# Kernel tuning notes

Measured on AMD Instinct MI355X. Metric: run time of the kernel, lower is better.

## Reference

```python
import jax, jax.numpy as jnp
import numpy as np

EMBED_DIM = 512
N_HEADS = 8
HEAD_DIM = EMBED_DIM // N_HEADS
B, N = 4, 2048


def setup_inputs() -> dict:
    key = jax.random.key(0)
    ks = jax.random.split(key, 5)
    x = jax.random.normal(ks[0], (B, N, EMBED_DIM), dtype=jnp.float32)
    # torch Linear weights are (out, in); init scale ~ 1/sqrt(in)
    s = 1.0 / np.sqrt(EMBED_DIM)
    WQ = jax.random.uniform(ks[1], (EMBED_DIM, EMBED_DIM), jnp.float32, -s, s)
    WK = jax.random.uniform(ks[2], (EMBED_DIM, EMBED_DIM), jnp.float32, -s, s)
    WV = jax.random.uniform(ks[3], (EMBED_DIM, EMBED_DIM), jnp.float32, -s, s)
    WO = jax.random.uniform(ks[4], (EMBED_DIM, EMBED_DIM), jnp.float32, -s, s)
    mask = jnp.tril(jnp.ones((N, N), dtype=jnp.int32))  # causal mask
    return {"x": x, "WQ": WQ, "WK": WK, "WV": WV, "WO": WO, "mask": mask}


def reference(x, WQ, WK, WV, WO, mask):
    scale = HEAD_DIM ** -0.5
    # Linear: y = x @ W.T ; then split heads -> (B, H, N, Dh)
    def proj(W):
        y = jnp.einsum('bnd,ed->bne', x, W)
        return y.reshape(B, N, N_HEADS, HEAD_DIM).transpose(0, 2, 1, 3)
    Q, K, V = proj(WQ), proj(WK), proj(WV)
    scores = jnp.einsum('bhnd,bhmd->bhnm', Q, K) * scale  # (B,H,N,N)
    scores = jnp.where(mask[None, None, :, :] == 0, -jnp.inf, scores)
    attn = jax.nn.softmax(scores, axis=-1)
    # dropout is identity in eval mode
    out = jnp.einsum('bhnm,bhmd->bhnd', attn, V)
    out = out.transpose(0, 2, 1, 3).reshape(B, N, EMBED_DIM)
    return jnp.einsum('bne,de->bnd', out, WO)
```

## Files before the change

### kernel.cpp

```cpp
#include <hip/hip_runtime.h>
#include <hip/hip_bf16.h>

#define B_  4
#define N_  2048
#define E_  512
#define H_  8
#define DH_ 64
#define M_  (B_ * N_)

typedef __attribute__((ext_vector_type(8))) short bq8;
typedef __attribute__((ext_vector_type(4))) float f32x4;

#define QSCALE_ (0.125f * 1.44269504f)

static __device__ __forceinline__ unsigned short f2bf(float f) {
    unsigned u = __float_as_uint(f);
    unsigned r = (u + 0x7fffu + ((u >> 16) & 1u)) >> 16;
    return (unsigned short)r;
}
static __device__ __forceinline__ unsigned short f2bf_fast(float f) {
    return (unsigned short)((__float_as_uint(f) + 0x8000u) >> 16);
}

static __device__ __forceinline__ void gld_lds16(const unsigned short* g,
                                                 unsigned short* l)
{
    __builtin_amdgcn_global_load_lds(
        (const __attribute__((address_space(1))) void*)g,
        (__attribute__((address_space(3))) void*)l,
        16, 0, 0);
}

static __device__ __forceinline__ void cvt16(const void* src, unsigned short* dst,
                                             int base, bool isBf)
{
    if (isBf) {
        const uint4* s = (const uint4*)((const unsigned short*)src + base);
        uint4 a = s[0], b = s[1];
        *(uint4*)(dst + base)     = a;
        *(uint4*)(dst + base + 8) = b;
    } else {
        const float* s = (const float*)src + base;
        unsigned short tmp[16];
        #pragma unroll
        for (int c = 0; c < 16; c += 4) {
            const float4 v = *(const float4*)(s + c);
            tmp[c + 0] = f2bf(v.x); tmp[c + 1] = f2bf(v.y);
            tmp[c + 2] = f2bf(v.z); tmp[c + 3] = f2bf(v.w);
        }
        *(uint4*)(dst + base)     = *(uint4*)&tmp[0];
        *(uint4*)(dst + base + 8) = *(uint4*)&tmp[8];
    }
}

__global__ __launch_bounds__(256)
void cvt_all(const void* __restrict__ sx,
             const void* __restrict__ s0, const void* __restrict__ s1,
             const void* __restrict__ s2, const void* __restrict__ s3,
             unsigned short* __restrict__ dx,
             unsigned short* __restrict__ d0, unsigned short* __restrict__ d1,
             unsigned short* __restrict__ d2, unsigned short* __restrict__ d3,
             int* __restrict__ dflag)
{
    __shared__ int wtot[4];
    const int bid = blockIdx.x;
    const int t   = threadIdx.x;
    const void* s;
    unsigned short* d;
    int base;
    if (bid < 1024) {
        s = sx; d = dx;
        base = bid * 4096 + t * 16;
    } else {
        const int wb = bid - 1024;
        const int wi = wb >> 6;
        s = (wi == 0) ? s0 : (wi == 1) ? s1 : (wi == 2) ? s2 : s3;
        d = (wi == 0) ? d0 : (wi == 1) ? d1 : (wi == 2) ? d2 : d3;
        base = (wb & 63) * 4096 + t * 16;
    }

    const unsigned* sw = (const unsigned*)s;
    int cnt = 0;
    #pragma unroll
    for (int i = 0; i < 4; ++i) {
        const unsigned w = sw[t * 4 + i];
        const unsigned elo = (w >> 7) & 0xffu;
        const unsigned ehi = (w >> 23) & 0xffu;
        cnt += (elo >= 100u && elo <= 150u && ehi >= 100u && ehi <= 150u) ? 1 : 0;
    }
    cnt += __shfl_xor(cnt, 1);  cnt += __shfl_xor(cnt, 2);
    cnt += __shfl_xor(cnt, 4);  cnt += __shfl_xor(cnt, 8);
    cnt += __shfl_xor(cnt, 16); cnt += __shfl_xor(cnt, 32);
    if ((t & 63) == 0) wtot[t >> 6] = cnt;
    __syncthreads();
    const int total = wtot[0] + wtot[1] + wtot[2] + wtot[3];
    const bool isBf = (total >= 512);
    if (bid == 0 && t == 0) dflag[0] = isBf ? 1 : 0;

    cvt16(s, d, base, isBf);
}

template<int BN>
__global__ __launch_bounds__(256)
void gemm_bf16(const unsigned short* __restrict__ A,
               const unsigned short* __restrict__ W0,
               const unsigned short* __restrict__ W1,
               const unsigned short* __restrict__ W2,
               void* __restrict__ C0, void* __restrict__ C1, void* __restrict__ C2,
               const int* __restrict__ dflag, int cSel)
{
    constexpr int NB = BN / 32;
    __shared__ unsigned short As[128 * 32];
    __shared__ unsigned short Bs[BN * 32];

    const int extBf = dflag[0];
    const unsigned short* Wv = (blockIdx.z == 0) ? W0 : (blockIdx.z == 1) ? W1 : W2;
    void*                 Cv = (blockIdx.z == 0) ? C0 : (blockIdx.z == 1) ? C1 : C2;
    const int  mode  = (cSel == 1) ? 1 : ((blockIdx.z == 2) ? 2 : 0);
    const bool vswap = (mode == 2);
    const float qs = (cSel == 0 && blockIdx.z == 0) ? QSCALE_ : 1.0f;

    const int t    = threadIdx.x;
    const int w    = t >> 6;
    const int lane = t & 63;
    const int ln   = lane & 15;
    const int qd   = lane >> 4;
    const int wm   = w >> 1;
    const int wn   = w & 1;

    const int m0 = blockIdx.x * 128;
    const int n0 = blockIdx.y * BN;

    const int lr = lane >> 2;
    const int lc = (lane & 3) * 8;
    const unsigned short* gA0 = A + (size_t)(m0 + w * 32 + lr) * E_ + lc;
    const unsigned short* gA1 = gA0 + 16 * E_;
    unsigned short* lA0 = As + w * 32 * 32;
    unsigned short* lA1 = lA0 + 16 * 32;

    const unsigned short* gB0;
    const unsigned short* gB1 = nullptr;
    unsigned short* lB0;
    unsigned short* lB1 = nullptr;
    if (BN == 128) {
        gB0 = Wv + (size_t)(n0 + w * 32 + lr) * E_ + lc;
        gB1 = gB0 + 16 * E_;
        lB0 = Bs + w * 32 * 32;
        lB1 = lB0 + 16 * 32;
    } else {
        gB0 = Wv + (size_t)(n0 + w * 16 + lr) * E_ + lc;
        lB0 = Bs + w * 16 * 32;
    }

    f32x4 acc[4][4];
    #pragma unroll
    for (int i = 0; i < 4; ++i)
        #pragma unroll
        for (int j = 0; j < 4; ++j)
            acc[i][j] = (f32x4){0.f, 0.f, 0.f, 0.f};

    for (int k0 = 0; k0 < E_; k0 += 32) {
        __syncthreads();
        gld_lds16(gA0 + k0, lA0);
        gld_lds16(gA1 + k0, lA1);
        gld_lds16(gB0 + k0, lB0);
        if (BN == 128) gld_lds16(gB1 + k0, lB1);
        __syncthreads();

        bq8 afr[4], bfr[NB];
        #pragma unroll
        for (int i = 0; i < 4; ++i)
            afr[i] = *(const bq8*)&As[(wm * 64 + i * 16 + ln) * 32 + qd * 8];
        #pragma unroll
        for (int j = 0; j < NB; ++j)
            bfr[j] = *(const bq8*)&Bs[(wn * (BN / 2) + j * 16 + ln) * 32 + qd * 8];

        if (vswap) {
            #pragma unroll
            for (int i = 0; i < 4; ++i)
                #pragma unroll
                for (int j = 0; j < NB; ++j)
                    acc[i][j] = __builtin_amdgcn_mfma_f32_16x16x32_bf16(afr[i], bfr[j], acc[i][j], 0, 0, 0);
        } else {
            #pragma unroll
            for (int i = 0; i < NB; ++i)
                #pragma unroll
                for (int j = 0; j < 4; ++j)
                    acc[i][j] = __builtin_amdgcn_mfma_f32_16x16x32_bf16(bfr[i], afr[j], acc[i][j], 0, 0, 0);
        }
    }

    if (mode == 2) {
        unsigned short* C = (unsigned short*)Cv;
        const int colBase = n0 + wn * 64;
        const int hh = colBase >> 6;
        #pragma unroll
        for (int i = 0; i < 4; ++i) {
            const int token = m0 + wm * 64 + i * 16 + qd * 4;
            const int bb = token >> 11;
            const int nn = token & 2047;
            #pragma unroll
            for (int j = 0; j < 4; ++j) {
                const int d = j * 16 + ln;
                ushort4 o4;
                o4.x = f2bf(acc[i][j][0]);
                o4.y = f2bf(acc[i][j][1]);
                o4.z = f2bf(acc[i][j][2]);
                o4.w = f2bf(acc[i][j][3]);
                *(ushort4*)(C + ((size_t)(bb * H_ + hh) * 64 + d) * N_ + nn) = o4;
            }
        }
    } else if (mode == 0 || extBf) {
        unsigned short* C = (unsigned short*)Cv;
        #pragma unroll
        for (int i = 0; i < NB; ++i) {
            const int n = n0 + wn * (BN / 2) + i * 16 + qd * 4;
            #pragma unroll
            for (int j = 0; j < 4; ++j) {
                const int m = m0 + wm * 64 + j * 16 + ln;
                ushort4 o4;
                o4.x = f2bf(acc[i][j][0] * qs);
                o4.y = f2bf(acc[i][j][1] * qs);
                o4.z = f2bf(acc[i][j][2] * qs);
                o4.w = f2bf(acc[i][j][3] * qs);
                *(ushort4*)(C + (size_t)m * E_ + n) = o4;
            }
        }
    } else {
        float* C = (float*)Cv;
        #pragma unroll
        for (int i = 0; i < NB; ++i) {
            const int n = n0 + wn * (BN / 2) + i * 16 + qd * 4;
            #pragma unroll
            for (int j = 0; j < 4; ++j) {
                const int m = m0 + wm * 64 + j * 16 + ln;
                *(f32x4*)(C + (size_t)m * E_ + n) = acc[i][j];
            }
        }
    }
}

__global__ __launch_bounds__(256)
void attn_causal(const unsigned short* __restrict__ Q,
                 const unsigned short* __restrict__ K,
                 const unsigned short* __restrict__ VtG,
                 unsigned short* __restrict__ O)
{
    __shared__ unsigned short Ks[128 * 72];
    __shared__ unsigned short Vs[64 * 136];
    __shared__ unsigned short Pq[64 * 264];

    const int bx  = blockIdx.x;
    const int qlo = bx;
    const int qhi = 31 - bx;
    const int h   = blockIdx.y;
    const int b   = blockIdx.z;
    const int t   = threadIdx.x;
    const int w    = t >> 6;
    const int lane = t & 63;
    const int ln   = lane & 15;
    const int qd   = lane >> 4;

    const int CA = (qlo + 2) >> 1;
    const int CB = (qhi + 2) >> 1;

    const int col0 = h * DH_;
    const size_t rowBase = (size_t)b * N_;
    const unsigned short* Vhead = VtG + (size_t)(b * H_ + h) * 64 * N_;

    const int jbase = qd * 4;
    const int mloc  = w * 16 + ln;
    const int qAg = qlo * 64 + mloc;
    const int qBg = qhi * 64 + mloc;
    const int prow = mloc * 264;

    const unsigned short* Qa = Q + (rowBase + qAg) * E_ + col0 + qd * 8;
    const unsigned short* Qb = Q + (rowBase + qBg) * E_ + col0 + qd * 8;
    const bq8 qfA0 = *(const bq8*)(Qa);
    const bq8 qfA1 = *(const bq8*)(Qa + 32);
    const bq8 qfB0 = *(const bq8*)(Qb);
    const bq8 qfB1 = *(const bq8*)(Qb + 32);

    const int kr = t >> 1;
    const int kc = (t & 1) * 32;
    const int vr = t >> 2;
    const int vc = (t & 3) * 32;
    const unsigned short* gK = K + (rowBase + kr) * E_ + col0 + kc;
    const unsigned short* gV = Vhead + (size_t)vr * N_ + vc;

    float lA = 0.f, lB = 0.f;
    f32x4 oA[4], oB[4];
    #pragma unroll
    for (int dt = 0; dt < 4; ++dt) {
        oA[dt] = (f32x4){0.f, 0.f, 0.f, 0.f};
        oB[dt] = (f32x4){0.f, 0.f, 0.f, 0.f};
    }

    uint4 kR0, kR1, kR2, kR3, vR0, vR1, vR2, vR3;
    {
        const uint4* ks = (const uint4*)gK;
        kR0 = ks[0]; kR1 = ks[1]; kR2 = ks[2]; kR3 = ks[3];
        const uint4* vs = (const uint4*)gV;
        vR0 = vs[0]; vR1 = vs[1]; vR2 = vs[2]; vR3 = vs[3];
    }

    for (int kt = 0; kt < CB; ++kt) {
        const bool actA = (kt < CA);

        __syncthreads();
        *(uint4*)&Ks[kr * 72 + kc]      = kR0;
        *(uint4*)&Ks[kr * 72 + kc + 8]  = kR1;
        *(uint4*)&Ks[kr * 72 + kc + 16] = kR2;
        *(uint4*)&Ks[kr * 72 + kc + 24] = kR3;
        *(uint4*)&Vs[vr * 136 + vc]      = vR0;
        *(uint4*)&Vs[vr * 136 + vc + 8]  = vR1;
        *(uint4*)&Vs[vr * 136 + vc + 16] = vR2;
        *(uint4*)&Vs[vr * 136 + vc + 24] = vR3;
        __syncthreads();

        if (kt + 1 < CB) {
            const uint4* ks = (const uint4*)(gK + (size_t)(kt + 1) * 128 * E_);
            kR0 = ks[0]; kR1 = ks[1]; kR2 = ks[2]; kR3 = ks[3];
            const uint4* vs = (const uint4*)(gV + (kt + 1) * 128);
            vR0 = vs[0]; vR1 = vs[1]; vR2 = vs[2]; vR3 = vs[3];
        }

        const int gb = kt * 128 + jbase;

        f32x4 sA[8];
        const bool diagB = (kt == CB - 1);
        #pragma unroll
        for (int ct = 0; ct < 8; ++ct) {
            const bq8 kf0 = *(const bq8*)&Ks[(ct * 16 + ln) * 72 + qd * 8];
            const bq8 kf1 = *(const bq8*)&Ks[(ct * 16 + ln) * 72 + 32 + qd * 8];
            f32x4 c = (f32x4){0.f, 0.f, 0.f, 0.f};
            c = __builtin_amdgcn_mfma_f32_16x16x32_bf16(kf0, qfB0, c, 0, 0, 0);
            c = __builtin_amdgcn_mfma_f32_16x16x32_bf16(kf1, qfB1, c, 0, 0, 0);
            if (actA) {
                f32x4 ca = (f32x4){0.f, 0.f, 0.f, 0.f};
                ca = __builtin_amdgcn_mfma_f32_16x16x32_bf16(kf0, qfA0, ca, 0, 0, 0);
                ca = __builtin_amdgcn_mfma_f32_16x16x32_bf16(kf1, qfA1, ca, 0, 0, 0);
                sA[ct] = ca;
            }
            float p0 = exp2f(c[0]);
            float p1 = exp2f(c[1]);
            float p2 = exp2f(c[2]);
            float p3 = exp2f(c[3]);
            if (diagB) {
                const int kb = gb + ct * 16;
                if (kb + 0 > qBg) p0 = 0.f;
                if (kb + 1 > qBg) p1 = 0.f;
                if (kb + 2 > qBg) p2 = 0.f;
                if (kb + 3 > qBg) p3 = 0.f;
            }
            lB += (p0 + p1) + (p2 + p3);
            ushort4 pk;
            pk.x = f2bf_fast(p0); pk.y = f2bf_fast(p1);
            pk.z = f2bf_fast(p2); pk.w = f2bf_fast(p3);
            *(ushort4*)&Pq[prow + 136 + ct * 16 + jbase] = pk;
        }

        if (actA) {
            const bool diagA = (kt == CA - 1);
            #pragma unroll
            for (int ct = 0; ct < 8; ++ct) {
                float p0 = exp2f(sA[ct][0]);
                float p1 = exp2f(sA[ct][1]);
                float p2 = exp2f(sA[ct][2]);
                float p3 = exp2f(sA[ct][3]);
                if (diagA) {
                    const int kb = gb + ct * 16;
                    if (kb + 0 > qAg) p0 = 0.f;
                    if (kb + 1 > qAg) p1 = 0.f;
                    if (kb + 2 > qAg) p2 = 0.f;
                    if (kb + 3 > qAg) p3 = 0.f;
                }
                lA += (p0 + p1) + (p2 + p3);
                ushort4 pk;
                pk.x = f2bf_fast(p0); pk.y = f2bf_fast(p1);
                pk.z = f2bf_fast(p2); pk.w = f2bf_fast(p3);
                *(ushort4*)&Pq[prow + ct * 16 + jbase] = pk;
            }
        }

        {
            const bq8 pB0 = *(const bq8*)&Pq[prow + 136 + qd * 8];
            const bq8 pB1 = *(const bq8*)&Pq[prow + 136 + 32 + qd * 8];
            const bq8 pB2 = *(const bq8*)&Pq[prow + 136 + 64 + qd * 8];
            const bq8 pB3 = *(const bq8*)&Pq[prow + 136 + 96 + qd * 8];
            bq8 pA0, pA1, pA2, pA3;
            if (actA) {
                pA0 = *(const bq8*)&Pq[prow + qd * 8];
                pA1 = *(const bq8*)&Pq[prow + 32 + qd * 8];
                pA2 = *(const bq8*)&Pq[prow + 64 + qd * 8];
                pA3 = *(const bq8*)&Pq[prow + 96 + qd * 8];
            }
            __builtin_amdgcn_s_setprio(1);
            #pragma unroll
            for (int dt = 0; dt < 4; ++dt) {
                const int vb = (dt * 16 + ln) * 136;
                const bq8 vf0 = *(const bq8*)&Vs[vb + qd * 8];
                const bq8 vf1 = *(const bq8*)&Vs[vb + 32 + qd * 8];
                const bq8 vf2 = *(const bq8*)&Vs[vb + 64 + qd * 8];
                const bq8 vf3 = *(const bq8*)&Vs[vb + 96 + qd * 8];
                oB[dt] = __builtin_amdgcn_mfma_f32_16x16x32_bf16(vf0, pB0, oB[dt], 0, 0, 0);
                oB[dt] = __builtin_amdgcn_mfma_f32_16x16x32_bf16(vf1, pB1, oB[dt], 0, 0, 0);
                oB[dt] = __builtin_amdgcn_mfma_f32_16x16x32_bf16(vf2, pB2, oB[dt], 0, 0, 0);
                oB[dt] = __builtin_amdgcn_mfma_f32_16x16x32_bf16(vf3, pB3, oB[dt], 0, 0, 0);
                if (actA) {
                    oA[dt] = __builtin_amdgcn_mfma_f32_16x16x32_bf16(vf0, pA0, oA[dt], 0, 0, 0);
                    oA[dt] = __builtin_amdgcn_mfma_f32_16x16x32_bf16(vf1, pA1, oA[dt], 0, 0, 0);
                    oA[dt] = __builtin_amdgcn_mfma_f32_16x16x32_bf16(vf2, pA2, oA[dt], 0, 0, 0);
                    oA[dt] = __builtin_amdgcn_mfma_f32_16x16x32_bf16(vf3, pA3, oA[dt], 0, 0, 0);
                }
            }
            __builtin_amdgcn_s_setprio(0);
        }
    }

    lA += __shfl_xor(lA, 16); lA += __shfl_xor(lA, 32);
    lB += __shfl_xor(lB, 16); lB += __shfl_xor(lB, 32);
    const float invA = 1.f / lA;
    const float invB = 1.f / lB;

    unsigned short* oAp = O + (rowBase + qlo * 64 + mloc) * E_ + col0 + jbase;
    unsigned short* oBp = O + (rowBase + qhi * 64 + mloc) * E_ + col0 + jbase;
    #pragma unroll
    for (int dt = 0; dt < 4; ++dt) {
        ushort4 a4, b4;
        a4.x = f2bf(oA[dt][0] * invA); a4.y = f2bf(oA[dt][1] * invA);
        a4.z = f2bf(oA[dt][2] * invA); a4.w = f2bf(oA[dt][3] * invA);
        b4.x = f2bf(oB[dt][0] * invB); b4.y = f2bf(oB[dt][1] * invB);
        b4.z = f2bf(oB[dt][2] * invB); b4.w = f2bf(oB[dt][3] * invB);
        *(ushort4*)(oAp + dt * 16) = a4;
        *(ushort4*)(oBp + dt * 16) = b4;
    }
}

extern "C" void kernel_launch(void* const* d_in, const int* in_sizes, int n_in,
                              void* d_out, int out_size, void* d_ws, size_t ws_size,
                              hipStream_t stream)
{
    const void* x  = d_in[0];
    const void* WQ = d_in[1];
    const void* WK = d_in[2];
    const void* WV = d_in[3];
    const void* WO = d_in[4];

    int* dflag = (int*)d_ws;
    unsigned short* xb  = (unsigned short*)((char*)d_ws + 256);
    unsigned short* wqb = xb  + (size_t)M_ * E_;
    unsigned short* wkb = wqb + (size_t)E_ * E_;
    unsigned short* wvb = wkb + (size_t)E_ * E_;
    unsigned short* wob = wvb + (size_t)E_ * E_;
    unsigned short* q   = wob + (size_t)E_ * E_;
    unsigned short* k   = q   + (size_t)M_ * E_;
    unsigned short* v   = k   + (size_t)M_ * E_;
    unsigned short* o   = v   + (size_t)M_ * E_;

    cvt_all<<<1280, 256, 0, stream>>>(x, WQ, WK, WV, WO,
                                      xb, wqb, wkb, wvb, wob, dflag);

    gemm_bf16<128><<<dim3(M_ / 128, E_ / 128, 3), 256, 0, stream>>>(
        xb, wqb, wkb, wvb, q, k, v, dflag, 0);

    attn_causal<<<dim3(16, H_, B_), 256, 0, stream>>>(q, k, v, o);

    gemm_bf16<64><<<dim3(M_ / 128, E_ / 64, 1), 256, 0, stream>>>(
        o, wob, wob, wob, d_out, d_out, d_out, dflag, 1);
}
```

Before: 197.3 us.

## Specialize causal attention loop into paired and B-only paths, share P buffer

Splits the key-tile loop of the paired-tile causal attention kernel into two branches. One handles tiles where both the low and high query tiles are active, the other handles tiles where only the high tile remains, which removes the per-instruction actA predicates and the live sA array. The P staging buffer in LDS is halved by writing and reading A's probabilities first, then reusing the same rows for B, which lowers shared-memory use per block. Manual bf16 rounding is replaced by the packed v_cvt_pk_bf16_f32 instruction. The intent is fewer instructions, lower register and LDS pressure, and possibly higher occupancy, at the cost of duplicated code and a serialized write/read of P within the active path.

After: 174.9 us. 11.4% less time.

```diff
diff --git a/kernel.cpp b/kernel.cpp
--- a/kernel.cpp
+++ b/kernel.cpp
@@ -18,8 +18,11 @@
     unsigned r = (u + 0x7fffu + ((u >> 16) & 1u)) >> 16;
     return (unsigned short)r;
 }
-static __device__ __forceinline__ unsigned short f2bf_fast(float f) {
-    return (unsigned short)((__float_as_uint(f) + 0x8000u) >> 16);
+
+static __device__ __forceinline__ unsigned cvtpk_bf16(float lo, float hi) {
+    unsigned r;
+    asm("v_cvt_pk_bf16_f32 %0, %1, %2" : "=v"(r) : "v"(lo), "v"(hi));
+    return r;
 }
 
 static __device__ __forceinline__ void gld_lds16(const unsigned short* g,
@@ -248,7 +251,7 @@
 {
     __shared__ unsigned short Ks[128 * 72];
     __shared__ unsigned short Vs[64 * 136];
-    __shared__ unsigned short Pq[64 * 264];
+    __shared__ unsigned short Pq[64 * 136];
 
     const int bx  = blockIdx.x;
     const int qlo = bx;
@@ -272,7 +275,7 @@
     const int mloc  = w * 16 + ln;
     const int qAg = qlo * 64 + mloc;
     const int qBg = qhi * 64 + mloc;
-    const int prow = mloc * 264;
+    const int prow = mloc * 136;
 
     const unsigned short* Qa = Q + (rowBase + qAg) * E_ + col0 + qd * 8;
     const unsigned short* Qb = Q + (rowBase + qBg) * E_ + col0 + qd * 8;
@@ -305,8 +308,6 @@
     }
 
     for (int kt = 0; kt < CB; ++kt) {
-        const bool actA = (kt < CA);
-
         __syncthreads();
         *(uint4*)&Ks[kr * 72 + kc]      = kR0;
         *(uint4*)&Ks[kr * 72 + kc + 8]  = kR1;
@@ -327,47 +328,24 @@
 
         const int gb = kt * 128 + jbase;
 
-        f32x4 sA[8];
-        const bool diagB = (kt == CB - 1);
-        #pragma unroll
-        for (int ct = 0; ct < 8; ++ct) {
-            const bq8 kf0 = *(const bq8*)&Ks[(ct * 16 + ln) * 72 + qd * 8];
-            const bq8 kf1 = *(const bq8*)&Ks[(ct * 16 + ln) * 72 + 32 + qd * 8];
-            f32x4 c = (f32x4){0.f, 0.f, 0.f, 0.f};
-            c = __builtin_amdgcn_mfma_f32_16x16x32_bf16(kf0, qfB0, c, 0, 0, 0);
-            c = __builtin_amdgcn_mfma_f32_16x16x32_bf16(kf1, qfB1, c, 0, 0, 0);
-            if (actA) {
+        if (kt < CA) {
+            const bool diagA = (kt == CA - 1);
+            f32x4 sB[8];
+            #pragma unroll
+            for (int ct = 0; ct < 8; ++ct) {
+                const bq8 kf0 = *(const bq8*)&Ks[(ct * 16 + ln) * 72 + qd * 8];
+                const bq8 kf1 = *(const bq8*)&Ks[(ct * 16 + ln) * 72 + 32 + qd * 8];
                 f32x4 ca = (f32x4){0.f, 0.f, 0.f, 0.f};
                 ca = __builtin_amdgcn_mfma_f32_16x16x32_bf16(kf0, qfA0, ca, 0, 0, 0);
                 ca = __builtin_amdgcn_mfma_f32_16x16x32_bf16(kf1, qfA1, ca, 0, 0, 0);
-                sA[ct] = ca;
-            }
-            float p0 = exp2f(c[0]);
-            float p1 = exp2f(c[1]);
-            float p2 = exp2f(c[2]);
-            float p3 = exp2f(c[3]);
-            if (diagB) {
-                const int kb = gb + ct * 16;
-                if (kb + 0 > qBg) p0 = 0.f;
-                if (kb + 1 > qBg) p1 = 0.f;
-                if (kb + 2 > qBg) p2 = 0.f;
-                if (kb + 3 > qBg) p3 = 0.f;
-            }
-            lB += (p0 + p1) + (p2 + p3);
-            ushort4 pk;
-            pk.x = f2bf_fast(p0); pk.y = f2bf_fast(p1);
-            pk.z = f2bf_fast(p2); pk.w = f2bf_fast(p3);
-            *(ushort4*)&Pq[prow + 136 + ct * 16 + jbase] = pk;
-        }
-
-        if (actA) {
-            const bool diagA = (kt == CA - 1);
-            #pragma unroll
-            for (int ct = 0; ct < 8; ++ct) {
-                float p0 = exp2f(sA[ct][0]);
-                float p1 = exp2f(sA[ct][1]);
-                float p2 = exp2f(sA[ct][2]);
-                float p3 = exp2f(sA[ct][3]);
+                f32x4 c = (f32x4){0.f, 0.f, 0.f, 0.f};
+                c = __builtin_amdgcn_mfma_f32_16x16x32_bf16(kf0, qfB0, c, 0, 0, 0);
+                c = __builtin_amdgcn_mfma_f32_16x16x32_bf16(kf1, qfB1, c, 0, 0, 0);
+                sB[ct] = c;
+                float p0 = exp2f(ca[0]);
+                float p1 = exp2f(ca[1]);
+                float p2 = exp2f(ca[2]);
+                float p3 = exp2f(ca[3]);
                 if (diagA) {
                     const int kb = gb + ct * 16;
                     if (kb + 0 > qAg) p0 = 0.f;
@@ -376,25 +354,33 @@
                     if (kb + 3 > qAg) p3 = 0.f;
                 }
                 lA += (p0 + p1) + (p2 + p3);
-                ushort4 pk;
-                pk.x = f2bf_fast(p0); pk.y = f2bf_fast(p1);
-                pk.z = f2bf_fast(p2); pk.w = f2bf_fast(p3);
-                *(ushort4*)&Pq[prow + ct * 16 + jbase] = pk;
-            }
-        }
-
-        {
-            const bq8 pB0 = *(const bq8*)&Pq[prow + 136 + qd * 8];
-            const bq8 pB1 = *(const bq8*)&Pq[prow + 136 + 32 + qd * 8];
-            const bq8 pB2 = *(const bq8*)&Pq[prow + 136 + 64 + qd * 8];
-            const bq8 pB3 = *(const bq8*)&Pq[prow + 136 + 96 + qd * 8];
-            bq8 pA0, pA1, pA2, pA3;
-            if (actA) {
-                pA0 = *(const bq8*)&Pq[prow + qd * 8];
-                pA1 = *(const bq8*)&Pq[prow + 32 + qd * 8];
-                pA2 = *(const bq8*)&Pq[prow + 64 + qd * 8];
-                pA3 = *(const bq8*)&Pq[prow + 96 + qd * 8];
-            }
+                uint2 pk2;
+                pk2.x = cvtpk_bf16(p0, p1);
+                pk2.y = cvtpk_bf16(p2, p3);
+                *(uint2*)&Pq[prow + ct * 16 + jbase] = pk2;
+            }
+            const bq8 pA0 = *(const bq8*)&Pq[prow + qd * 8];
+            const bq8 pA1 = *(const bq8*)&Pq[prow + 32 + qd * 8];
+            const bq8 pA2 = *(const bq8*)&Pq[prow + 64 + qd * 8];
+            const bq8 pA3 = *(const bq8*)&Pq[prow + 96 + qd * 8];
+
+            #pragma unroll
+            for (int ct = 0; ct < 8; ++ct) {
+                const float p0 = exp2f(sB[ct][0]);
+                const float p1 = exp2f(sB[ct][1]);
+                const float p2 = exp2f(sB[ct][2]);
+                const float p3 = exp2f(sB[ct][3]);
+                lB += (p0 + p1) + (p2 + p3);
+                uint2 pk2;
+                pk2.x = cvtpk_bf16(p0, p1);
+                pk2.y = cvtpk_bf16(p2, p3);
+                *(uint2*)&Pq[prow + ct * 16 + jbase] = pk2;
+            }
+            const bq8 pB0 = *(const bq8*)&Pq[prow + qd * 8];
+            const bq8 pB1 = *(const bq8*)&Pq[prow + 32 + qd * 8];
+            const bq8 pB2 = *(const bq8*)&Pq[prow + 64 + qd * 8];
+            const bq8 pB3 = *(const bq8*)&Pq[prow + 96 + qd * 8];
+
             __builtin_amdgcn_s_setprio(1);
             #pragma unroll
             for (int dt = 0; dt < 4; ++dt) {
@@ -407,12 +393,55 @@
                 oB[dt] = __builtin_amdgcn_mfma_f32_16x16x32_bf16(vf1, pB1, oB[dt], 0, 0, 0);
                 oB[dt] = __builtin_amdgcn_mfma_f32_16x16x32_bf16(vf2, pB2, oB[dt], 0, 0, 0);
                 oB[dt] = __builtin_amdgcn_mfma_f32_16x16x32_bf16(vf3, pB3, oB[dt], 0, 0, 0);
-                if (actA) {
-                    oA[dt] = __builtin_amdgcn_mfma_f32_16x16x32_bf16(vf0, pA0, oA[dt], 0, 0, 0);
-                    oA[dt] = __builtin_amdgcn_mfma_f32_16x16x32_bf16(vf1, pA1, oA[dt], 0, 0, 0);
-                    oA[dt] = __builtin_amdgcn_mfma_f32_16x16x32_bf16(vf2, pA2, oA[dt], 0, 0, 0);
-                    oA[dt] = __builtin_amdgcn_mfma_f32_16x16x32_bf16(vf3, pA3, oA[dt], 0, 0, 0);
+                oA[dt] = __builtin_amdgcn_mfma_f32_16x16x32_bf16(vf0, pA0, oA[dt], 0, 0, 0);
+                oA[dt] = __builtin_amdgcn_mfma_f32_16x16x32_bf16(vf1, pA1, oA[dt], 0, 0, 0);
+                oA[dt] = __builtin_amdgcn_mfma_f32_16x16x32_bf16(vf2, pA2, oA[dt], 0, 0, 0);
+                oA[dt] = __builtin_amdgcn_mfma_f32_16x16x32_bf16(vf3, pA3, oA[dt], 0, 0, 0);
+            }
+            __builtin_amdgcn_s_setprio(0);
+        } else {
+            const bool diagB = (kt == CB - 1);
+            #pragma unroll
+            for (int ct = 0; ct < 8; ++ct) {
+                const bq8 kf0 = *(const bq8*)&Ks[(ct * 16 + ln) * 72 + qd * 8];
+                const bq8 kf1 = *(const bq8*)&Ks[(ct * 16 + ln) * 72 + 32 + qd * 8];
+                f32x4 c = (f32x4){0.f, 0.f, 0.f, 0.f};
+                c = __builtin_amdgcn_mfma_f32_16x16x32_bf16(kf0, qfB0, c, 0, 0, 0);
+                c = __builtin_amdgcn_mfma_f32_16x16x32_bf16(kf1, qfB1, c, 0, 0, 0);
+                float p0 = exp2f(c[0]);
+                float p1 = exp2f(c[1]);
+                float p2 = exp2f(c[2]);
+                float p3 = exp2f(c[3]);
+                if (diagB) {
+                    const int kb = gb + ct * 16;
+                    if (kb + 0 > qBg) p0 = 0.f;
+                    if (kb + 1 > qBg) p1 = 0.f;
+                    if (kb + 2 > qBg) p2 = 0.f;
+                    if (kb + 3 > qBg) p3 = 0.f;
                 }
+                lB += (p0 + p1) + (p2 + p3);
+                uint2 pk2;
+                pk2.x = cvtpk_bf16(p0, p1);
+                pk2.y = cvtpk_bf16(p2, p3);
+                *(uint2*)&Pq[prow + ct * 16 + jbase] = pk2;
+            }
+            const bq8 pB0 = *(const bq8*)&Pq[prow + qd * 8];
+            const bq8 pB1 = *(const bq8*)&Pq[prow + 32 + qd * 8];
+            const bq8 pB2 = *(const bq8*)&Pq[prow + 64 + qd * 8];
+            const bq8 pB3 = *(const bq8*)&Pq[prow + 96 + qd * 8];
+
+            __builtin_amdgcn_s_setprio(1);
+            #pragma unroll
+            for (int dt = 0; dt < 4; ++dt) {
+                const int vb = (dt * 16 + ln) * 136;
+                const bq8 vf0 = *(const bq8*)&Vs[vb + qd * 8];
+                const bq8 vf1 = *(const bq8*)&Vs[vb + 32 + qd * 8];
+                const bq8 vf2 = *(const bq8*)&Vs[vb + 64 + qd * 8];
+                const bq8 vf3 = *(const bq8*)&Vs[vb + 96 + qd * 8];
+                oB[dt] = __builtin_amdgcn_mfma_f32_16x16x32_bf16(vf0, pB0, oB[dt], 0, 0, 0);
+                oB[dt] = __builtin_amdgcn_mfma_f32_16x16x32_bf16(vf1, pB1, oB[dt], 0, 0, 0);
+                oB[dt] = __builtin_amdgcn_mfma_f32_16x16x32_bf16(vf2, pB2, oB[dt], 0, 0, 0);
+                oB[dt] = __builtin_amdgcn_mfma_f32_16x16x32_bf16(vf3, pB3, oB[dt], 0, 0, 0);
             }
             __builtin_amdgcn_s_setprio(0);
         }
```
